# Kernel optimization log

Hardware: AMD Instinct MI355X
Metric: run time of the kernel (lower is better)

Reference implementation:

```python
import jax, jax.numpy as jnp
import numpy as np

B = 4096
FEAT = 512
EMB = 64
HID = 1024
NUM_CLASSES = 64   # == option_num == noise_lib_Y.shape[0]
LIB_X = 256
LIB_Y = 256
OUT_J = 256


def setup_inputs() -> dict:
    key = jax.random.key(0)
    ks = jax.random.split(key, 16)
    s = lambda k, shape, fan: jax.random.normal(k, shape, jnp.float32) / np.sqrt(fan)
    d_in = FEAT + EMB
    return {
        "state": jax.random.normal(ks[0], (B, FEAT), jnp.float32),
        "option": jax.random.randint(ks[1], (B,), 0, NUM_CLASSES, jnp.int64),
        "embed_table": s(ks[2], (NUM_CLASSES, EMB), EMB),
        "Wx1": s(ks[3], (d_in, HID), d_in), "bx1": jnp.zeros((HID,), jnp.float32),
        "Wx2": s(ks[4], (HID, LIB_X), HID), "bx2": jnp.zeros((LIB_X,), jnp.float32),
        "Wy1": s(ks[5], (d_in, HID), d_in), "by1": jnp.zeros((HID,), jnp.float32),
        "Wy2": s(ks[6], (HID, LIB_Y), HID), "by2": jnp.zeros((LIB_Y,), jnp.float32),
        "noise_lib_X": s(ks[7], (LIB_X, OUT_J), LIB_X),
        "noise_lib_Y": s(ks[8], (NUM_CLASSES, LIB_Y, OUT_J), LIB_Y),
    }


def _mlp(x, W1, b1, W2, b2):
    # MLP_RELU, layer_num=2: Linear -> ReLU -> Linear
    h = jax.nn.relu(x @ W1 + b1)
    return h @ W2 + b2


def reference(state, option, embed_table, Wx1, bx1, Wx2, bx2,
              Wy1, by1, Wy2, by2, noise_lib_X, noise_lib_Y):
    option_embed = embed_table[option]                      # [B, EMB]
    all_state = jnp.concatenate([state, option_embed], axis=-1)
    cls_X = _mlp(all_state, Wx1, bx1, Wx2, bx2)             # [B, LIB_X]
    cls_Y = _mlp(all_state, Wy1, by1, Wy2, by2)             # [B, LIB_Y]
    # Original: einsum('bi,mij->bmj') then mask with one_hot(option).
    # Mathematically identical gather-then-matmul (honors the routing sparsity):
    noise_Y_sel = noise_lib_Y[option]                       # [B, LIB_Y, OUT_J]
    generate_noise_Y = jnp.einsum('bi,bij->bj', cls_Y, noise_Y_sel)
    generate_noise_X = cls_X @ noise_lib_X                  # [B, OUT_J]
    return (generate_noise_X, generate_noise_Y)
```

## Files before the change

kernel.cpp:

```cpp
#include <hip/hip_runtime.h>

typedef unsigned short u16;
typedef unsigned int u32;

using f32x4  = __attribute__((ext_vector_type(4))) float;
using bf16x8 = __attribute__((ext_vector_type(8))) __bf16;

#define DEV __device__ __forceinline__

DEV u16 f2bf(float f) {
  union { float f; u32 u; } x; x.f = f;
  return (u16)((x.u + 0x7fffu + ((x.u >> 16) & 1u)) >> 16);
}
DEV float bf2f(u16 h) {
  union { u32 u; float f; } x; x.u = ((u32)h) << 16;
  return x.f;
}

DEV void async_cp16(const u16* g, u16* l) {
  __builtin_amdgcn_global_load_lds((const __attribute__((address_space(1))) void*)g,
                                   (__attribute__((address_space(3))) void*)l,
                                   16, 0, 0);
}

static constexpr int BATCH = 4096;
static constexpr int FEAT  = 512;
static constexpr int EMB   = 64;
static constexpr int HID   = 1024;
static constexpr int NC    = 64;
static constexpr int DIN   = 576;
static constexpr int LIB   = 256;

DEV void detect_lite(const u32* __restrict__ sraw, const u32* __restrict__ oraw,
                     int* isf32, int* ostr) {
  __shared__ int cib, conz;
  const int t = threadIdx.x;
  if (t == 0) { cib = 0; conz = 0; }
  u32 w = sraw[t];
  u32 e = (w >> 7) & 0xFFu;
  unsigned long long m1 = __ballot(e >= 100 && e <= 142);
  unsigned long long m2 = __ballot((t & 1) && oraw[t] != 0);
  __syncthreads();
  if ((t & 63) == 0) {
    atomicAdd(&cib, __popcll(m1));
    atomicAdd(&conz, __popcll(m2));
  }
  __syncthreads();
  *isf32 = (cib < 128) ? 1 : 0;
  *ostr  = (conz == 0) ? 2 : 1;
}

DEV void load16_bf(u16* v, const void* __restrict__ in, size_t off, int isf32) {
  if (isf32) {
    const float4* s = (const float4*)((const float*)in + off);
    float4 a0 = s[0], a1 = s[1], a2 = s[2], a3 = s[3];
    v[0] = f2bf(a0.x); v[1] = f2bf(a0.y); v[2]  = f2bf(a0.z); v[3]  = f2bf(a0.w);
    v[4] = f2bf(a1.x); v[5] = f2bf(a1.y); v[6]  = f2bf(a1.z); v[7]  = f2bf(a1.w);
    v[8] = f2bf(a2.x); v[9] = f2bf(a2.y); v[10] = f2bf(a2.z); v[11] = f2bf(a2.w);
    v[12] = f2bf(a3.x); v[13] = f2bf(a3.y); v[14] = f2bf(a3.z); v[15] = f2bf(a3.w);
  } else {
    const uint4* s = (const uint4*)((const u16*)in + off);
    *(uint4*)&v[0] = s[0];
    *(uint4*)&v[8] = s[1];
  }
}

DEV void do_transpose64(u16* lds, const void* __restrict__ in,
                        u16* __restrict__ out, int R, int C,
                        int by, int bx, int isf32) {
  u16* tile = lds;
  const int t = threadIdx.x;
  {
    const int r = t >> 2, c0 = (t & 3) * 16;
    u16 v[16];
    load16_bf(v, in, (size_t)(by * 64 + r) * C + (bx * 64 + c0), isf32);
    *(uint4*)&tile[r * 72 + c0]     = *(uint4*)&v[0];
    *(uint4*)&tile[r * 72 + c0 + 8] = *(uint4*)&v[8];
  }
  __syncthreads();
  {
    const int c = t & 63, rs = (t >> 6) * 16;
    u16 w[16];
#pragma unroll
    for (int i = 0; i < 16; ++i) w[i] = tile[(rs + i) * 72 + c];
    size_t oo = (size_t)(bx * 64 + c) * R + (by * 64 + rs);
    *(uint4*)&out[oo]     = *(uint4*)&w[0];
    *(uint4*)&out[oo + 8] = *(uint4*)&w[8];
  }
}

DEV void tgemm_task(u16* lds, const void* __restrict__ nX,
                    const void* __restrict__ Wx2, u16* __restrict__ T,
                    int mt, int nt, int isf32) {
  u16* Als = lds;
  u16* Bls = lds + 64 * 72;
  const int t = threadIdx.x;
  const int m0 = mt * 64, q0 = nt * 64;
  const int lane = t & 63, wid = t >> 6;
  const int wm = wid >> 1, wn = wid & 1;
  const int lr = lane & 15, lq = lane >> 4;
  f32x4 acc[2][2] = {};
  for (int k0 = 0; k0 < LIB; k0 += 64) {
    __syncthreads();
    {
      const int r = t >> 2, c0 = (t & 3) * 16;
      u16 v[16];
      load16_bf(v, nX, (size_t)(k0 + r) * LIB + m0 + c0, isf32);
#pragma unroll
      for (int j = 0; j < 16; ++j) Als[(c0 + j) * 72 + r] = v[j];
      const int q = t >> 2, ic = (t & 3) * 16;
      u16 w16[16];
      load16_bf(w16, Wx2, (size_t)(q0 + q) * LIB + k0 + ic, isf32);
      u16* dst = &Bls[((ic >> 5) * 64 + q) * 32 + (ic & 31)];
      *(uint4*)dst       = *(uint4*)&w16[0];
      *(uint4*)(dst + 8) = *(uint4*)&w16[8];
    }
    __syncthreads();
#pragma unroll
    for (int sl = 0; sl < 2; ++sl) {
      bf16x8 av[2], bv[2];
#pragma unroll
      for (int i2 = 0; i2 < 2; ++i2)
        av[i2] = *(const bf16x8*)&Als[(wm * 32 + i2 * 16 + lr) * 72 + sl * 32 + lq * 8];
#pragma unroll
      for (int j2 = 0; j2 < 2; ++j2)
        bv[j2] = *(const bf16x8*)&Bls[(sl * 64 + wn * 32 + j2 * 16 + lr) * 32 + lq * 8];
#pragma unroll
      for (int i2 = 0; i2 < 2; ++i2)
#pragma unroll
        for (int j2 = 0; j2 < 2; ++j2)
          acc[i2][j2] = __builtin_amdgcn_mfma_f32_16x16x32_bf16(av[i2], bv[j2], acc[i2][j2], 0, 0, 0);
    }
  }
#pragma unroll
  for (int j2 = 0; j2 < 2; ++j2) {
    const int gc = q0 + wn * 32 + j2 * 16 + lr;
#pragma unroll
    for (int i2 = 0; i2 < 2; ++i2) {
      const int gr = m0 + wm * 32 + i2 * 16 + lq * 4;
#pragma unroll
      for (int r = 0; r < 4; ++r)
        T[(size_t)(gr + r) * HID + gc] = f2bf(acc[i2][j2][r]);
    }
  }
}

struct PrepArgs {
  const void *state, *emb, *Wx1, *Wy1;
  const int* opt;
  u16 *all_state, *WT1x, *WT1y;
};
static constexpr int PB_CONCAT = BATCH * 36 / 256;
static constexpr int PB_WT1 = (DIN / 64) * (HID / 64);
static constexpr int PREP_BLOCKS = PB_CONCAT + 2 * PB_WT1;

__global__ __launch_bounds__(256) void prep_k(PrepArgs a) {
  __shared__ __align__(16) u16 plds[64 * 72];
  int isf32, os;
  detect_lite((const u32*)a.state, (const u32*)a.opt, &isf32, &os);
  int bid = blockIdx.x;
  const int t = threadIdx.x;
  if (bid < PB_CONCAT) {
    int idx = bid * 256 + t;
    int b = idx / 36, ch = idx % 36;
    const void* base;
    size_t srcoff;
    if (ch < 32) { base = a.state; srcoff = (size_t)b * FEAT + ch * 16; }
    else {
      base = a.emb;
      srcoff = (size_t)a.opt[(size_t)b * os] * EMB + (ch - 32) * 16;
    }
    u16 o[16];
    load16_bf(o, base, srcoff, isf32);
    u16* dst = a.all_state + (size_t)b * DIN + ch * 16;
    *(uint4*)dst       = *(const uint4*)&o[0];
    *(uint4*)(dst + 8) = *(const uint4*)&o[8];
    return;
  }
  bid -= PB_CONCAT;
  if (bid < PB_WT1) { do_transpose64(plds, a.Wx1, a.WT1x, DIN, HID, bid >> 4, bid & 15, isf32); return; }
  bid -= PB_WT1;
  do_transpose64(plds, a.Wy1, a.WT1y, DIN, HID, bid >> 4, bid & 15, isf32);
}

template <int BM, int BN, int SLABS, bool RELU>
DEV void gemm_tile(u16* lds, const u16* __restrict__ A, const u16* __restrict__ Bt,
                   const void* bias, void* C, int N, int K, int m0, int n0,
                   int isf32, bool cf32, bool bf32) {
  constexpr int WM = BM / 2, WN = BN / 2, TM = WM / 16, TN = WN / 16;
  constexpr int BUFE = (BM + BN) * 32 * SLABS;
  const int t = threadIdx.x;
  const int lane = t & 63, wid = t >> 6;
  const int wm = wid >> 1, wn = wid & 1;
  const int lr = lane & 15, lq = lane >> 4;

  auto stage = [&](int buf, int k0) {
    u16* As = lds + buf * BUFE;
    u16* Bs = As + BM * 32 * SLABS;
#pragma unroll
    for (int sl = 0; sl < SLABS; ++sl) {
#pragma unroll
      for (int u = 0; u < BM / 64; ++u) {
        int unit = u * 256 + t;
        int r = unit >> 2, c8 = (unit & 3) * 8;
        async_cp16(A + (size_t)(m0 + r) * K + (k0 + sl * 32 + c8),
                   &As[(sl * BM + r) * 32 + c8]);
      }
#pragma unroll
      for (int u = 0; u < BN / 64; ++u) {
        int unit = u * 256 + t;
        int r = unit >> 2, c8 = (unit & 3) * 8;
        async_cp16(Bt + (size_t)(n0 + r) * K + (k0 + sl * 32 + c8),
                   &Bs[(sl * BN + r) * 32 + c8]);
      }
    }
  };

  f32x4 acc[TM][TN] = {};
  stage(0, 0);
  __syncthreads();
  int cur = 0;
  for (int k0 = 0; k0 < K; k0 += 32 * SLABS) {
    const int kn = k0 + 32 * SLABS;
    if (kn < K) stage(cur ^ 1, kn);
    const u16* As = lds + cur * BUFE;
    const u16* Bs = As + BM * 32 * SLABS;
#pragma unroll
    for (int sl = 0; sl < SLABS; ++sl) {
      bf16x8 av[TM], bv[TN];
#pragma unroll
      for (int i = 0; i < TM; ++i)
        av[i] = *(const bf16x8*)&As[(sl * BM + wm * WM + i * 16 + lr) * 32 + lq * 8];
#pragma unroll
      for (int j = 0; j < TN; ++j)
        bv[j] = *(const bf16x8*)&Bs[(sl * BN + wn * WN + j * 16 + lr) * 32 + lq * 8];
#pragma unroll
      for (int i = 0; i < TM; ++i)
#pragma unroll
        for (int j = 0; j < TN; ++j)
          acc[i][j] = __builtin_amdgcn_mfma_f32_16x16x32_bf16(av[i], bv[j], acc[i][j], 0, 0, 0);
    }
    __syncthreads();
    cur ^= 1;
  }
#pragma unroll
  for (int j = 0; j < TN; ++j) {
    const int gc = n0 + wn * WN + j * 16 + lr;
    const float bval = bias
        ? (bf32 ? ((const float*)bias)[gc] : bf2f(((const u16*)bias)[gc]))
        : 0.f;
#pragma unroll
    for (int i = 0; i < TM; ++i) {
      const int gr = m0 + wm * WM + i * 16 + lq * 4;
#pragma unroll
      for (int r = 0; r < 4; ++r) {
        float v = acc[i][j][r] + bval;
        if (RELU) v = fmaxf(v, 0.f);
        const size_t idx = (size_t)(gr + r) * N + gc;
        if (cf32) ((float*)C)[idx] = v;
        else      ((u16*)C)[idx] = f2bf(v);
      }
    }
  }
}

struct G1Args {
  const u16 *all_state, *WT1x, *WT1y;
  const void *bx1, *by1, *Wy2, *nX, *Wx2, *bx2, *state, *opt;
  u16 *h_x, *h_y, *WT2y, *T;
  float* b2x;
};
static constexpr int G1_GEMM = 512;
static constexpr int G1_BLOCKS = G1_GEMM + 64 + 64 + 4;

__global__ __launch_bounds__(256) void gemm1_k(G1Args a) {
  __shared__ __align__(16) u16 lds[2 * (128 + 128) * 32 * 2];
  __shared__ float red[4][64];
  int isf32, os;
  detect_lite((const u32*)a.state, (const u32*)a.opt, &isf32, &os);
  int bid = blockIdx.x;
  const int t = threadIdx.x;
  if (bid < G1_GEMM) {
    const int x = bid & 7, y = (bid >> 3) & 31, z = bid >> 8;
    gemm_tile<128, 128, 2, true>(lds,
        a.all_state, z ? a.WT1y : a.WT1x, z ? a.by1 : a.bx1,
        z ? a.h_y : a.h_x, HID, DIN, y * 128, x * 128, isf32, false, isf32);
    return;
  }
  bid -= G1_GEMM;
  if (bid < 64) { do_transpose64(lds, a.Wy2, a.WT2y, HID, LIB, bid >> 2, bid & 3, isf32); return; }
  bid -= 64;
  if (bid < 64) { tgemm_task(lds, a.nX, a.Wx2, a.T, bid & 3, bid >> 2, isf32); return; }
  bid -= 64;
  {
    const int j = bid * 64 + (t & 63), g = t >> 6;
    float acc = 0.f;
    for (int ii = 0; ii < 64; ++ii) {
      const int i = g * 64 + ii;
      float s = isf32 ? ((const float*)a.bx2)[i] : bf2f(((const u16*)a.bx2)[i]);
      float v = isf32 ? ((const float*)a.nX)[(size_t)i * LIB + j]
                      : bf2f(((const u16*)a.nX)[(size_t)i * LIB + j]);
      acc += s * v;
    }
    red[g][t & 63] = acc;
    __syncthreads();
    if (g == 0)
      a.b2x[j] = red[0][t & 63] + red[1][t & 63] + red[2][t & 63] + red[3][t & 63];
  }
}

struct GArg { const u16* A; const u16* Bt; const void* bias; void* C; int cflag; int bflag; };

template <int BM, int BN, int SLABS, bool RELU>
__global__ __launch_bounds__(256) void gemm_bt(GArg g0, GArg g1, int N, int K,
                                               const void* state, const void* opt) {
  __shared__ __align__(16) u16 lds[2 * (BM + BN) * 32 * SLABS];
  int isf32, os;
  detect_lite((const u32*)state, (const u32*)opt, &isf32, &os);
  const GArg g = blockIdx.z ? g1 : g0;
  gemm_tile<BM, BN, SLABS, RELU>(lds, g.A, g.Bt, g.bias, g.C, N, K,
                                 blockIdx.y * BM, blockIdx.x * BN,
                                 isf32, g.cflag && isf32, g.bflag || isf32);
}

struct TailArgs {
  const u16* cls_y;
  const void *nY, *state;
  const int* opt;
  void* out;
};

static constexpr int TSTR = 266;

__global__ __launch_bounds__(256) void tail_k(TailArgs a) {
  __shared__ __align__(16) u16 lds[25216];
  __shared__ int lcnt;
  int isf32, os;
  detect_lite((const u32*)a.state, (const u32*)a.opt, &isf32, &os);
  const bool of32 = (isf32 != 0);
  const int t = threadIdx.x;
  const int lane = t & 63, w = t >> 6, lr = lane & 15, lq = lane >> 4;

  u16* Bts  = lds;
  u16* Asm  = lds + 64 * TSTR;
  u16* list = lds + 80 * TSTR;
  const int m = blockIdx.x >> 3;
  const int n0 = ((blockIdx.x >> 1) & 3) * 64;
  const int half = blockIdx.x & 1;
  if (t == 0) lcnt = 0;

#pragma unroll
  for (int pass = 0; pass < 4; ++pass) {
    const int k = pass * 64 + (t >> 2), nc = (t & 3) * 16;
    u16 v[16];
    load16_bf(v, a.nY, ((size_t)m * LIB + k) * LIB + n0 + nc, isf32);
#pragma unroll
    for (int j = 0; j < 16; ++j) Bts[(nc + j) * TSTR + k] = v[j];
  }

  __syncthreads();
  const int bstart = half * (BATCH / 2), bend = bstart + BATCH / 2;
  for (int base = bstart; base < bend; base += 256) {
    const int b = base + t;
    const int e = a.opt[(size_t)b * os];
    unsigned long long mk = __ballot(e == m);
    const int nw = __popcll(mk);
    int wbase = 0;
    if (lane == 0 && nw) wbase = atomicAdd(&lcnt, nw);
    wbase = __shfl(wbase, 0);
    const int mypre = __popcll(mk & ((1ull << lane) - 1ull));
    if (e == m) list[wbase + mypre] = (u16)b;
  }
  __syncthreads();
  const int cnt = lcnt;
  const size_t out_off = (size_t)BATCH * LIB;

  for (int ch = 0; ch < cnt; ch += 16) {
    __syncthreads();
    {
      const int r = t >> 4, cb = (t & 15) * 16;
      if (ch + r < cnt) {
        const u16* src = a.cls_y + (size_t)list[ch + r] * LIB + cb;
        *(uint4*)&Asm[r * TSTR + cb]     = *(const uint4*)src;
        *(uint4*)&Asm[r * TSTR + cb + 8] = *(const uint4*)(src + 8);
      } else {
        uint4 z{0, 0, 0, 0};
        *(uint4*)&Asm[r * TSTR + cb]     = z;
        *(uint4*)&Asm[r * TSTR + cb + 8] = z;
      }
    }
    __syncthreads();
    f32x4 acc = {};
#pragma unroll
    for (int kk = 0; kk < LIB; kk += 32) {
      bf16x8 av = *(const bf16x8*)&Asm[lr * TSTR + kk + lq * 8];
      bf16x8 bv = *(const bf16x8*)&Bts[(w * 16 + lr) * TSTR + kk + lq * 8];
      acc = __builtin_amdgcn_mfma_f32_16x16x32_bf16(av, bv, acc, 0, 0, 0);
    }
#pragma unroll
    for (int r = 0; r < 4; ++r) {
      const int rowc = lq * 4 + r;
      if (ch + rowc < cnt) {
        const size_t oi = out_off + (size_t)list[ch + rowc] * LIB
                        + (n0 + w * 16 + lr);
        if (of32) ((float*)a.out)[oi] = acc[r];
        else      ((u16*)a.out)[oi] = f2bf(acc[r]);
      }
    }
  }
}

extern "C" void kernel_launch(void* const* d_in, const int* in_sizes, int n_in,
                              void* d_out, int out_size, void* d_ws, size_t ws_size,
                              hipStream_t stream) {
  char* p = (char*)d_ws;
  auto alloc = [&](size_t bytes) { char* r = p; p += (bytes + 255) & ~(size_t)255; return r; };
  u16* all_state = (u16*)alloc((size_t)BATCH * DIN * 2);
  u16* h_x   = (u16*)alloc((size_t)BATCH * HID * 2);
  u16* h_y   = (u16*)alloc((size_t)BATCH * HID * 2);
  u16* cls_y = (u16*)alloc((size_t)BATCH * LIB * 2);
  u16* WT1x  = (u16*)alloc((size_t)HID * DIN * 2);
  u16* WT1y  = (u16*)alloc((size_t)HID * DIN * 2);
  u16* WT2y  = (u16*)alloc((size_t)LIB * HID * 2);
  u16* T     = (u16*)alloc((size_t)LIB * HID * 2);
  float* b2x = (float*)alloc((size_t)LIB * 4);

  const void* state = d_in[0];
  const void* opt   = d_in[1];

  PrepArgs pa;
  pa.state = state; pa.opt = (const int*)opt; pa.emb = d_in[2];
  pa.Wx1 = d_in[3]; pa.Wy1 = d_in[7];
  pa.all_state = all_state; pa.WT1x = WT1x; pa.WT1y = WT1y;
  prep_k<<<PREP_BLOCKS, 256, 0, stream>>>(pa);

  G1Args g1;
  g1.all_state = all_state; g1.WT1x = WT1x; g1.WT1y = WT1y;
  g1.bx1 = d_in[4]; g1.by1 = d_in[8];
  g1.Wy2 = d_in[9]; g1.nX = d_in[11]; g1.Wx2 = d_in[5]; g1.bx2 = d_in[6];
  g1.state = state; g1.opt = opt;
  g1.h_x = h_x; g1.h_y = h_y; g1.WT2y = WT2y; g1.T = T; g1.b2x = b2x;
  gemm1_k<<<G1_BLOCKS, 256, 0, stream>>>(g1);

  GArg g2x{h_x, T, b2x, d_out, 1, 1};
  GArg g2y{h_y, WT2y, d_in[10], cls_y, 0, 0};
  gemm_bt<64, 64, 4, false><<<dim3(LIB / 64, BATCH / 64, 2), 256, 0, stream>>>(
      g2x, g2y, LIB, HID, state, opt);

  TailArgs ta{cls_y, d_in[12], state, (const int*)opt, d_out};
  tail_k<<<512, 256, 0, stream>>>(ta);
}
```

Measured before the change: 159.4 us.

## Precompute per-class embedding projection and shrink first-layer GEMM K to FEAT

The embedding part of the first layer is split off algebraically. A per-class table E = emb @ W1[FEAT:] + b1 (64 x HID) is computed in the prep kernel and added in the GEMM epilogue by indexing on each row's option. This removes the concat buffer and cuts the first GEMM's K from 576 to 512. The weight transposes and T/b2x precompute also move into prep. The first GEMM becomes a 512-thread 128x128 tile, and both GEMMs drop LDS double-buffering in favour of single-buffered load-sync-compute, which can expose global load latency.

New measurement: 153.3 us. 1.04x faster.

```diff
diff --git a/kernel.cpp b/kernel.cpp
--- a/kernel.cpp
+++ b/kernel.cpp
@@ -145,154 +145,109 @@
   }
 }
 
-struct PrepArgs {
-  const void *state, *emb, *Wx1, *Wy1;
-  const int* opt;
-  u16 *all_state, *WT1x, *WT1y;
-};
-static constexpr int PB_CONCAT = BATCH * 36 / 256;
-static constexpr int PB_WT1 = (DIN / 64) * (HID / 64);
-static constexpr int PREP_BLOCKS = PB_CONCAT + 2 * PB_WT1;
-
-__global__ __launch_bounds__(256) void prep_k(PrepArgs a) {
-  __shared__ __align__(16) u16 plds[64 * 72];
-  int isf32, os;
-  detect_lite((const u32*)a.state, (const u32*)a.opt, &isf32, &os);
-  int bid = blockIdx.x;
-  const int t = threadIdx.x;
-  if (bid < PB_CONCAT) {
-    int idx = bid * 256 + t;
-    int b = idx / 36, ch = idx % 36;
-    const void* base;
-    size_t srcoff;
-    if (ch < 32) { base = a.state; srcoff = (size_t)b * FEAT + ch * 16; }
-    else {
-      base = a.emb;
-      srcoff = (size_t)a.opt[(size_t)b * os] * EMB + (ch - 32) * 16;
-    }
-    u16 o[16];
-    load16_bf(o, base, srcoff, isf32);
-    u16* dst = a.all_state + (size_t)b * DIN + ch * 16;
-    *(uint4*)dst       = *(const uint4*)&o[0];
-    *(uint4*)(dst + 8) = *(const uint4*)&o[8];
-    return;
-  }
-  bid -= PB_CONCAT;
-  if (bid < PB_WT1) { do_transpose64(plds, a.Wx1, a.WT1x, DIN, HID, bid >> 4, bid & 15, isf32); return; }
-  bid -= PB_WT1;
-  do_transpose64(plds, a.Wy1, a.WT1y, DIN, HID, bid >> 4, bid & 15, isf32);
-}
-
-template <int BM, int BN, int SLABS, bool RELU>
-DEV void gemm_tile(u16* lds, const u16* __restrict__ A, const u16* __restrict__ Bt,
-                   const void* bias, void* C, int N, int K, int m0, int n0,
-                   int isf32, bool cf32, bool bf32) {
-  constexpr int WM = BM / 2, WN = BN / 2, TM = WM / 16, TN = WN / 16;
-  constexpr int BUFE = (BM + BN) * 32 * SLABS;
-  const int t = threadIdx.x;
+DEV void etask(u16* lds, const void* __restrict__ emb, const void* __restrict__ W1,
+               const void* __restrict__ b1, float* __restrict__ E,
+               int nt, int isf32) {
+  u16* Als = lds;
+  u16* Bls = lds + 64 * 72;
+  const int t = threadIdx.x;
+  const int n0 = nt * 64;
   const int lane = t & 63, wid = t >> 6;
   const int wm = wid >> 1, wn = wid & 1;
   const int lr = lane & 15, lq = lane >> 4;
-
-  auto stage = [&](int buf, int k0) {
-    u16* As = lds + buf * BUFE;
-    u16* Bs = As + BM * 32 * SLABS;
-#pragma unroll
-    for (int sl = 0; sl < SLABS; ++sl) {
-#pragma unroll
-      for (int u = 0; u < BM / 64; ++u) {
-        int unit = u * 256 + t;
-        int r = unit >> 2, c8 = (unit & 3) * 8;
-        async_cp16(A + (size_t)(m0 + r) * K + (k0 + sl * 32 + c8),
-                   &As[(sl * BM + r) * 32 + c8]);
-      }
-#pragma unroll
-      for (int u = 0; u < BN / 64; ++u) {
-        int unit = u * 256 + t;
-        int r = unit >> 2, c8 = (unit & 3) * 8;
-        async_cp16(Bt + (size_t)(n0 + r) * K + (k0 + sl * 32 + c8),
-                   &Bs[(sl * BN + r) * 32 + c8]);
-      }
-    }
-  };
-
-  f32x4 acc[TM][TN] = {};
-  stage(0, 0);
+  {
+    const int r = t >> 2, c0 = (t & 3) * 16;
+    u16 v[16];
+    load16_bf(v, emb, (size_t)r * EMB + c0, isf32);
+    *(uint4*)&Als[r * 72 + c0]     = *(uint4*)&v[0];
+    *(uint4*)&Als[r * 72 + c0 + 8] = *(uint4*)&v[8];
+    u16 w16[16];
+    load16_bf(w16, W1, (size_t)(FEAT + r) * HID + n0 + c0, isf32);
+#pragma unroll
+    for (int j = 0; j < 16; ++j) Bls[(c0 + j) * 72 + r] = w16[j];
+  }
   __syncthreads();
-  int cur = 0;
-  for (int k0 = 0; k0 < K; k0 += 32 * SLABS) {
-    const int kn = k0 + 32 * SLABS;
-    if (kn < K) stage(cur ^ 1, kn);
-    const u16* As = lds + cur * BUFE;
-    const u16* Bs = As + BM * 32 * SLABS;
-#pragma unroll
-    for (int sl = 0; sl < SLABS; ++sl) {
-      bf16x8 av[TM], bv[TN];
-#pragma unroll
-      for (int i = 0; i < TM; ++i)
-        av[i] = *(const bf16x8*)&As[(sl * BM + wm * WM + i * 16 + lr) * 32 + lq * 8];
-#pragma unroll
-      for (int j = 0; j < TN; ++j)
-        bv[j] = *(const bf16x8*)&Bs[(sl * BN + wn * WN + j * 16 + lr) * 32 + lq * 8];
-#pragma unroll
-      for (int i = 0; i < TM; ++i)
-#pragma unroll
-        for (int j = 0; j < TN; ++j)
-          acc[i][j] = __builtin_amdgcn_mfma_f32_16x16x32_bf16(av[i], bv[j], acc[i][j], 0, 0, 0);
-    }
-    __syncthreads();
-    cur ^= 1;
-  }
-#pragma unroll
-  for (int j = 0; j < TN; ++j) {
-    const int gc = n0 + wn * WN + j * 16 + lr;
-    const float bval = bias
-        ? (bf32 ? ((const float*)bias)[gc] : bf2f(((const u16*)bias)[gc]))
-        : 0.f;
-#pragma unroll
-    for (int i = 0; i < TM; ++i) {
-      const int gr = m0 + wm * WM + i * 16 + lq * 4;
-#pragma unroll
-      for (int r = 0; r < 4; ++r) {
-        float v = acc[i][j][r] + bval;
-        if (RELU) v = fmaxf(v, 0.f);
-        const size_t idx = (size_t)(gr + r) * N + gc;
-        if (cf32) ((float*)C)[idx] = v;
-        else      ((u16*)C)[idx] = f2bf(v);
-      }
-    }
-  }
-}
-
-struct G1Args {
-  const u16 *all_state, *WT1x, *WT1y;
-  const void *bx1, *by1, *Wy2, *nX, *Wx2, *bx2, *state, *opt;
-  u16 *h_x, *h_y, *WT2y, *T;
-  float* b2x;
+  f32x4 acc[2][2] = {};
+#pragma unroll
+  for (int sl = 0; sl < 2; ++sl) {
+    bf16x8 av[2], bv[2];
+#pragma unroll
+    for (int i2 = 0; i2 < 2; ++i2)
+      av[i2] = *(const bf16x8*)&Als[(wm * 32 + i2 * 16 + lr) * 72 + sl * 32 + lq * 8];
+#pragma unroll
+    for (int j2 = 0; j2 < 2; ++j2)
+      bv[j2] = *(const bf16x8*)&Bls[(wn * 32 + j2 * 16 + lr) * 72 + sl * 32 + lq * 8];
+#pragma unroll
+    for (int i2 = 0; i2 < 2; ++i2)
+#pragma unroll
+      for (int j2 = 0; j2 < 2; ++j2)
+        acc[i2][j2] = __builtin_amdgcn_mfma_f32_16x16x32_bf16(av[i2], bv[j2], acc[i2][j2], 0, 0, 0);
+  }
+#pragma unroll
+  for (int j2 = 0; j2 < 2; ++j2) {
+    const int gc = n0 + wn * 32 + j2 * 16 + lr;
+    const float bval = isf32 ? ((const float*)b1)[gc] : bf2f(((const u16*)b1)[gc]);
+#pragma unroll
+    for (int i2 = 0; i2 < 2; ++i2) {
+      const int gr = wm * 32 + i2 * 16 + lq * 4;
+#pragma unroll
+      for (int r = 0; r < 4; ++r)
+        E[(size_t)(gr + r) * HID + gc] = acc[i2][j2][r] + bval;
+    }
+  }
+}
+
+struct PrepArgs {
+  const void *state, *emb, *Wx1, *Wy1, *bx1, *by1;
+  const void *Wy2, *nX, *Wx2, *bx2;
+  const int* opt;
+  u16 *state_bf, *WT1x, *WT1y, *WT2y, *T;
+  float *b2x, *Ex, *Ey;
 };
-static constexpr int G1_GEMM = 512;
-static constexpr int G1_BLOCKS = G1_GEMM + 64 + 64 + 4;
-
-__global__ __launch_bounds__(256) void gemm1_k(G1Args a) {
-  __shared__ __align__(16) u16 lds[2 * (128 + 128) * 32 * 2];
+static constexpr int PB_COPY = 512;
+static constexpr int PB_WT1  = (FEAT / 64) * (HID / 64);
+static constexpr int PB_WT2  = 64;
+static constexpr int PB_TG   = 64;
+static constexpr int PB_B2   = 4;
+static constexpr int PB_E    = 32;
+static constexpr int PREP_BLOCKS =
+    PB_COPY + 2 * PB_WT1 + PB_WT2 + PB_TG + PB_B2 + PB_E;
+
+__global__ __launch_bounds__(256) void prep_k(PrepArgs a) {
+  __shared__ __align__(16) u16 plds[2 * 64 * 72];
   __shared__ float red[4][64];
   int isf32, os;
   detect_lite((const u32*)a.state, (const u32*)a.opt, &isf32, &os);
   int bid = blockIdx.x;
   const int t = threadIdx.x;
-  if (bid < G1_GEMM) {
-    const int x = bid & 7, y = (bid >> 3) & 31, z = bid >> 8;
-    gemm_tile<128, 128, 2, true>(lds,
-        a.all_state, z ? a.WT1y : a.WT1x, z ? a.by1 : a.bx1,
-        z ? a.h_y : a.h_x, HID, DIN, y * 128, x * 128, isf32, false, isf32);
+  if (bid < PB_COPY) {
+    const size_t off = ((size_t)bid * 256 + t) * 16;
+    u16 o[16];
+    load16_bf(o, a.state, off, isf32);
+    u16* dst = a.state_bf + off;
+    *(uint4*)dst       = *(const uint4*)&o[0];
+    *(uint4*)(dst + 8) = *(const uint4*)&o[8];
     return;
   }
-  bid -= G1_GEMM;
-  if (bid < 64) { do_transpose64(lds, a.Wy2, a.WT2y, HID, LIB, bid >> 2, bid & 3, isf32); return; }
-  bid -= 64;
-  if (bid < 64) { tgemm_task(lds, a.nX, a.Wx2, a.T, bid & 3, bid >> 2, isf32); return; }
-  bid -= 64;
-  {
+  bid -= PB_COPY;
+  if (bid < PB_WT1) {
+    do_transpose64(plds, a.Wx1, a.WT1x, FEAT, HID, bid >> 4, bid & 15, isf32);
+    return;
+  }
+  bid -= PB_WT1;
+  if (bid < PB_WT1) {
+    do_transpose64(plds, a.Wy1, a.WT1y, FEAT, HID, bid >> 4, bid & 15, isf32);
+    return;
+  }
+  bid -= PB_WT1;
+  if (bid < PB_WT2) {
+    do_transpose64(plds, a.Wy2, a.WT2y, HID, LIB, bid >> 2, bid & 3, isf32);
+    return;
+  }
+  bid -= PB_WT2;
+  if (bid < PB_TG) { tgemm_task(plds, a.nX, a.Wx2, a.T, bid & 3, bid >> 2, isf32); return; }
+  bid -= PB_TG;
+  if (bid < PB_B2) {
     const int j = bid * 64 + (t & 63), g = t >> 6;
     float acc = 0.f;
     for (int ii = 0; ii < 64; ++ii) {
@@ -306,6 +261,152 @@
     __syncthreads();
     if (g == 0)
       a.b2x[j] = red[0][t & 63] + red[1][t & 63] + red[2][t & 63] + red[3][t & 63];
+    return;
+  }
+  bid -= PB_B2;
+  {
+    const int z = bid >> 4, nt = bid & 15;
+    etask(plds, a.emb, z ? a.Wy1 : a.Wx1, z ? a.by1 : a.bx1,
+          z ? a.Ey : a.Ex, nt, isf32);
+  }
+}
+
+struct G1Args {
+  const u16 *A, *WT1x, *WT1y;
+  const float *Ex, *Ey;
+  const void *state, *opt;
+  u16 *h_x, *h_y;
+};
+
+__global__ __launch_bounds__(512) void gemm1_k(G1Args a) {
+  constexpr int BM = 128, BN = 128, BK = 64, K = FEAT;
+  __shared__ __align__(16) u16 lds[(BM + BN) * BK];
+  int isf32, os;
+  detect_lite((const u32*)a.state, (const u32*)a.opt, &isf32, &os);
+  const int t = threadIdx.x;
+  const int lane = t & 63, wid = t >> 6;
+  const int wm = wid >> 2, wn = wid & 3;
+  const int lr = lane & 15, lq = lane >> 4;
+  const int m0 = blockIdx.y * BM, n0 = blockIdx.x * BN;
+  const u16* Bt = blockIdx.z ? a.WT1y : a.WT1x;
+  const float* E = blockIdx.z ? a.Ey : a.Ex;
+  u16* C = blockIdx.z ? a.h_y : a.h_x;
+  u16* As = lds;
+  u16* Bs = lds + BM * BK;
+  f32x4 acc[4][2] = {};
+  for (int k0 = 0; k0 < K; k0 += BK) {
+    __syncthreads();
+    {
+      const int r = t >> 2, c8 = (t & 3) * 8;
+#pragma unroll
+      for (int sl = 0; sl < 2; ++sl) {
+        async_cp16(a.A + (size_t)(m0 + r) * K + (k0 + sl * 32 + c8),
+                   &As[(sl * BM + r) * 32 + c8]);
+        async_cp16(Bt + (size_t)(n0 + r) * K + (k0 + sl * 32 + c8),
+                   &Bs[(sl * BN + r) * 32 + c8]);
+      }
+    }
+    __syncthreads();
+#pragma unroll
+    for (int sl = 0; sl < 2; ++sl) {
+      bf16x8 av[4], bv[2];
+#pragma unroll
+      for (int i = 0; i < 4; ++i)
+        av[i] = *(const bf16x8*)&As[(sl * BM + wm * 64 + i * 16 + lr) * 32 + lq * 8];
+#pragma unroll
+      for (int j = 0; j < 2; ++j)
+        bv[j] = *(const bf16x8*)&Bs[(sl * BN + wn * 32 + j * 16 + lr) * 32 + lq * 8];
+#pragma unroll
+      for (int i = 0; i < 4; ++i)
+#pragma unroll
+        for (int j = 0; j < 2; ++j)
+          acc[i][j] = __builtin_amdgcn_mfma_f32_16x16x32_bf16(av[i], bv[j], acc[i][j], 0, 0, 0);
+    }
+  }
+#pragma unroll
+  for (int i = 0; i < 4; ++i) {
+#pragma unroll
+    for (int r = 0; r < 4; ++r) {
+      const int gr = m0 + wm * 64 + i * 16 + lq * 4 + r;
+      const int cls = ((const int*)a.opt)[(size_t)gr * os];
+      const float* Erow = E + (size_t)cls * HID;
+#pragma unroll
+      for (int j = 0; j < 2; ++j) {
+        const int gc = n0 + wn * 32 + j * 16 + lr;
+        float v = acc[i][j][r] + Erow[gc];
+        v = fmaxf(v, 0.f);
+        C[(size_t)gr * HID + gc] = f2bf(v);
+      }
+    }
+  }
+}
+
+template <int BM, int BN, int SLABS, bool RELU>
+DEV void gemm_tile(u16* lds, const u16* __restrict__ A, const u16* __restrict__ Bt,
+                   const void* bias, void* C, int N, int K, int m0, int n0,
+                   int isf32, bool cf32, bool bf32) {
+  constexpr int WM = BM / 2, WN = BN / 2, TM = WM / 16, TN = WN / 16;
+  u16* As = lds;
+  u16* Bs = lds + BM * 32 * SLABS;
+  const int t = threadIdx.x;
+  const int lane = t & 63, wid = t >> 6;
+  const int wm = wid >> 1, wn = wid & 1;
+  const int lr = lane & 15, lq = lane >> 4;
+  f32x4 acc[TM][TN] = {};
+  for (int k0 = 0; k0 < K; k0 += 32 * SLABS) {
+    __syncthreads();
+#pragma unroll
+    for (int sl = 0; sl < SLABS; ++sl) {
+#pragma unroll
+      for (int u = 0; u < BM / 64; ++u) {
+        int unit = u * 256 + t;
+        int r = unit >> 2, c8 = (unit & 3) * 8;
+        async_cp16(A + (size_t)(m0 + r) * K + (k0 + sl * 32 + c8),
+                   &As[(sl * BM + r) * 32 + c8]);
+      }
+#pragma unroll
+      for (int u = 0; u < BN / 64; ++u) {
+        int unit = u * 256 + t;
+        int r = unit >> 2, c8 = (unit & 3) * 8;
+        async_cp16(Bt + (size_t)(n0 + r) * K + (k0 + sl * 32 + c8),
+                   &Bs[(sl * BN + r) * 32 + c8]);
+      }
+    }
+    __syncthreads();
+#pragma unroll
+    for (int sl = 0; sl < SLABS; ++sl) {
+      bf16x8 av[TM], bv[TN];
+#pragma unroll
+      for (int i = 0; i < TM; ++i)
+        av[i] = *(const bf16x8*)&As[(sl * BM + wm * WM + i * 16 + lr) * 32 + lq * 8];
+#pragma unroll
+      for (int j = 0; j < TN; ++j)
+        bv[j] = *(const bf16x8*)&Bs[(sl * BN + wn * WN + j * 16 + lr) * 32 + lq * 8];
+#pragma unroll
+      for (int i = 0; i < TM; ++i)
+#pragma unroll
+        for (int j = 0; j < TN; ++j)
+          acc[i][j] = __builtin_amdgcn_mfma_f32_16x16x32_bf16(av[i], bv[j], acc[i][j], 0, 0, 0);
+    }
+  }
+#pragma unroll
+  for (int j = 0; j < TN; ++j) {
+    const int gc = n0 + wn * WN + j * 16 + lr;
+    const float bval = bias
+        ? (bf32 ? ((const float*)bias)[gc] : bf2f(((const u16*)bias)[gc]))
+        : 0.f;
+#pragma unroll
+    for (int i = 0; i < TM; ++i) {
+      const int gr = m0 + wm * WM + i * 16 + lq * 4;
+#pragma unroll
+      for (int r = 0; r < 4; ++r) {
+        float v = acc[i][j][r] + bval;
+        if (RELU) v = fmaxf(v, 0.f);
+        const size_t idx = (size_t)(gr + r) * N + gc;
+        if (cf32) ((float*)C)[idx] = v;
+        else      ((u16*)C)[idx] = f2bf(v);
+      }
+    }
   }
 }
 
@@ -314,7 +415,7 @@
 template <int BM, int BN, int SLABS, bool RELU>
 __global__ __launch_bounds__(256) void gemm_bt(GArg g0, GArg g1, int N, int K,
                                                const void* state, const void* opt) {
-  __shared__ __align__(16) u16 lds[2 * (BM + BN) * 32 * SLABS];
+  __shared__ __align__(16) u16 lds[(BM + BN) * 32 * SLABS];
   int isf32, os;
   detect_lite((const u32*)state, (const u32*)opt, &isf32, &os);
   const GArg g = blockIdx.z ? g1 : g0;
@@ -415,32 +516,35 @@
                               hipStream_t stream) {
   char* p = (char*)d_ws;
   auto alloc = [&](size_t bytes) { char* r = p; p += (bytes + 255) & ~(size_t)255; return r; };
-  u16* all_state = (u16*)alloc((size_t)BATCH * DIN * 2);
+  u16* state_bf = (u16*)alloc((size_t)BATCH * FEAT * 2);
   u16* h_x   = (u16*)alloc((size_t)BATCH * HID * 2);
   u16* h_y   = (u16*)alloc((size_t)BATCH * HID * 2);
   u16* cls_y = (u16*)alloc((size_t)BATCH * LIB * 2);
-  u16* WT1x  = (u16*)alloc((size_t)HID * DIN * 2);
-  u16* WT1y  = (u16*)alloc((size_t)HID * DIN * 2);
+  u16* WT1x  = (u16*)alloc((size_t)HID * FEAT * 2);
+  u16* WT1y  = (u16*)alloc((size_t)HID * FEAT * 2);
   u16* WT2y  = (u16*)alloc((size_t)LIB * HID * 2);
   u16* T     = (u16*)alloc((size_t)LIB * HID * 2);
   float* b2x = (float*)alloc((size_t)LIB * 4);
+  float* Ex  = (float*)alloc((size_t)NC * HID * 4);
+  float* Ey  = (float*)alloc((size_t)NC * HID * 4);
 
   const void* state = d_in[0];
   const void* opt   = d_in[1];
 
   PrepArgs pa;
   pa.state = state; pa.opt = (const int*)opt; pa.emb = d_in[2];
-  pa.Wx1 = d_in[3]; pa.Wy1 = d_in[7];
-  pa.all_state = all_state; pa.WT1x = WT1x; pa.WT1y = WT1y;
+  pa.Wx1 = d_in[3]; pa.bx1 = d_in[4]; pa.Wy1 = d_in[7]; pa.by1 = d_in[8];
+  pa.Wy2 = d_in[9]; pa.nX = d_in[11]; pa.Wx2 = d_in[5]; pa.bx2 = d_in[6];
+  pa.state_bf = state_bf; pa.WT1x = WT1x; pa.WT1y = WT1y; pa.WT2y = WT2y;
+  pa.T = T; pa.b2x = b2x; pa.Ex = Ex; pa.Ey = Ey;
   prep_k<<<PREP_BLOCKS, 256, 0, stream>>>(pa);
 
   G1Args g1;
-  g1.all_state = all_state; g1.WT1x = WT1x; g1.WT1y = WT1y;
-  g1.bx1 = d_in[4]; g1.by1 = d_in[8];
-  g1.Wy2 = d_in[9]; g1.nX = d_in[11]; g1.Wx2 = d_in[5]; g1.bx2 = d_in[6];
+  g1.A = state_bf; g1.WT1x = WT1x; g1.WT1y = WT1y;
+  g1.Ex = Ex; g1.Ey = Ey;
   g1.state = state; g1.opt = opt;
-  g1.h_x = h_x; g1.h_y = h_y; g1.WT2y = WT2y; g1.T = T; g1.b2x = b2x;
-  gemm1_k<<<G1_BLOCKS, 256, 0, stream>>>(g1);
+  g1.h_x = h_x; g1.h_y = h_y;
+  gemm1_k<<<dim3(HID / 128, BATCH / 128, 2), 512, 0, stream>>>(g1);
 
   GArg g2x{h_x, T, b2x, d_out, 1, 1};
   GArg g2y{h_y, WT2y, d_in[10], cls_y, 0, 0};
```
